# Kernel optimization log

Measured on AMD Instinct MI355X. Metric: run time of the kernel, lower is better.

The kernel has to match this reference:

```python
import jax, jax.numpy as jnp
import numpy as np

EPS = 1e-12

def _l2normalize(v):
    return v / (jnp.sum(v ** 2) ** 0.5 + EPS)

def spectral_norm(w, u):
    # w: [Cin, Cout] (flattened 1x1 conv kernel), u: [1, Cout]; 1 power iteration
    v = _l2normalize(u @ w.T)          # [1, Cin]
    u2 = _l2normalize(v @ w)           # [1, Cout]
    sigma = (v @ w @ u2.T)[0, 0]
    return w / sigma

def conv1x1(x, w):
    # x: [B,H,W,Cin], w: [Cin,Cout]
    return jnp.einsum('bhwc,cd->bhwd', x, w)

def maxpool2(x):
    B, H, W, C = x.shape
    return x.reshape(B, H // 2, 2, W // 2, 2, C).max(axis=(2, 4))

def setup_inputs() -> dict:
    key = jax.random.key(0)
    ks = jax.random.split(key, 10)
    B, H, W, C = 16, 64, 64, 512
    c8, c2 = C // 8, C // 2
    x = jax.random.normal(ks[0], (B, H, W, C), dtype=jnp.float32)
    k_theta = jax.random.normal(ks[1], (C, c8), dtype=jnp.float32) * 0.05
    u_theta = jax.random.normal(ks[2], (1, c8), dtype=jnp.float32)
    k_phi = jax.random.normal(ks[3], (C, c8), dtype=jnp.float32) * 0.05
    u_phi = jax.random.normal(ks[4], (1, c8), dtype=jnp.float32)
    k_g = jax.random.normal(ks[5], (C, c2), dtype=jnp.float32) * 0.05
    u_g = jax.random.normal(ks[6], (1, c2), dtype=jnp.float32)
    k_attn = jax.random.normal(ks[7], (c2, C), dtype=jnp.float32) * 0.05
    u_attn = jax.random.normal(ks[8], (1, C), dtype=jnp.float32)
    sigma = jnp.float32(0.1)
    return {"x": x, "k_theta": k_theta, "u_theta": u_theta,
            "k_phi": k_phi, "u_phi": u_phi, "k_g": k_g, "u_g": u_g,
            "k_attn": k_attn, "u_attn": u_attn, "sigma": sigma}

def reference(x, k_theta, u_theta, k_phi, u_phi, k_g, u_g, k_attn, u_attn, sigma):
    B, H, W, C = x.shape
    c8, c2 = C // 8, C // 2
    loc = H * W
    down = loc // 4
    theta = conv1x1(x, spectral_norm(k_theta, u_theta)).reshape(B, loc, c8)
    phi = maxpool2(conv1x1(x, spectral_norm(k_phi, u_phi))).reshape(B, down, c8)
    attn = jax.nn.softmax(jnp.einsum('bnc,bmc->bnm', theta, phi), axis=-1)  # [B, loc, down]
    g = maxpool2(conv1x1(x, spectral_norm(k_g, u_g))).reshape(B, down, c2)
    attn_g = jnp.einsum('bnm,bmc->bnc', attn, g).reshape(B, H, W, c2)
    attn_g = conv1x1(attn_g, spectral_norm(k_attn, u_attn))
    return x + sigma * attn_g
```

## Files before the change

### kernel.cpp

```cpp
#include <hip/hip_runtime.h>
#include <hip/hip_bf16.h>


using bf16 = __hip_bfloat16;
typedef unsigned short u16;
typedef __attribute__((ext_vector_type(8))) short bf16x8;
typedef __attribute__((ext_vector_type(4))) float f32x4;

#define MFMA16(a, b, c) __builtin_amdgcn_mfma_f32_16x16x32_bf16((a), (b), (c), 0, 0, 0)

#define WS_FLAG   0
#define WS_WAT2   787456
#define WS_THETA  1311744
#define WS_PHI    9700352
#define WS_G      11797504
#define WS_WAT    20186112
#define WS_TOTAL  20448256

__device__ __forceinline__ float bf2f(bf16 v) { return __bfloat162float(v); }
__device__ __forceinline__ bf16 f2bf(float v) { return __float2bfloat16(v); }
__device__ __forceinline__ u16 f2bf_bits(float v) { bf16 h = f2bf(v); return *(u16*)&h; }

template <typename T> struct io;
template <> struct io<bf16> {
  static __device__ __forceinline__ float ld(const bf16* p) { return bf2f(*p); }
  static __device__ __forceinline__ void st(bf16* p, float v) { *p = f2bf(v); }
  static __device__ __forceinline__ int tag() { return 0; }
};
template <> struct io<float> {
  static __device__ __forceinline__ float ld(const float* p) { return *p; }
  static __device__ __forceinline__ void st(float* p, float v) { *p = v; }
  static __device__ __forceinline__ int tag() { return 1; }
};

__global__ __launch_bounds__(256) void detect_kernel(const void* xraw, int* flag) {
  const u16* p = (const u16*)xraw;
  int t = threadIdx.x;
  int cnt = 0;
  for (int i = t; i < 65536; i += 256) {
    u16 v = p[i];
    if ((v & 0x7F80u) == 0x7F80u) cnt++;
  }
#pragma unroll
  for (int o = 32; o > 0; o >>= 1) cnt += __shfl_down(cnt, o, 64);
  __shared__ int red[4];
  if ((t & 63) == 0) red[t >> 6] = cnt;
  __syncthreads();
  if (t == 0) flag[0] = (red[0] + red[1] + red[2] + red[3] > 4) ? 1 : 0;
}

__device__ __forceinline__ float block_sum_256(float x, float* red) {
#pragma unroll
  for (int o = 32; o > 0; o >>= 1) x += __shfl_down(x, o, 64);
  __syncthreads();
  if ((threadIdx.x & 63) == 0) red[threadIdx.x >> 6] = x;
  __syncthreads();
  return red[0] + red[1] + red[2] + red[3];
}

template <typename T>
__global__ __launch_bounds__(256) void sn_kernel(
    const void* ktv, const void* utv, const void* kpv, const void* upv,
    const void* kgv, const void* ugv, const void* kav, const void* uav,
    u16* wAllT, u16* waT, const int* flag) {
  if (flag[0] != io<T>::tag()) return;
  __shared__ float v[512];
  __shared__ float red[4];
  const T* w; const T* u; int cin, cout;
  switch (blockIdx.x) {
    case 0:  w = (const T*)ktv; u = (const T*)utv; cin = 512; cout = 64;  break;
    case 1:  w = (const T*)kpv; u = (const T*)upv; cin = 512; cout = 64;  break;
    case 2:  w = (const T*)kgv; u = (const T*)ugv; cin = 512; cout = 256; break;
    default: w = (const T*)kav; u = (const T*)uav; cin = 256; cout = 512; break;
  }
  int t = threadIdx.x;
  float loc = 0.f;
  for (int i = t; i < cin; i += 256) {
    float acc = 0.f;
    const T* wr = w + (size_t)i * cout;
    for (int j = 0; j < cout; ++j) acc += io<T>::ld(u + j) * io<T>::ld(wr + j);
    v[i] = acc;
    loc += acc * acc;
  }
  float s1 = block_sum_256(loc, red);
  float inv1 = 1.f / (sqrtf(s1) + 1e-12f);
  float loc2 = 0.f;
  for (int j = t; j < cout; j += 256) {
    float acc = 0.f;
    for (int i = 0; i < cin; ++i) acc += v[i] * io<T>::ld(w + (size_t)i * cout + j);
    acc *= inv1;
    loc2 += acc * acc;
  }
  float s2 = block_sum_256(loc2, red);
  float sigma = s2 / (sqrtf(s2) + 1e-12f);
  float winv = 1.f / sigma;
  int total = cin * cout;
  for (int k = t; k < total; k += 256) {
    float val = io<T>::ld(w + k) * winv;
    u16 bits = f2bf_bits(val);
    switch (blockIdx.x) {
      case 0:  wAllT[(size_t)((k & 63)) * 512 + (k >> 6)] = bits; break;
      case 1:  wAllT[(size_t)(64 + (k & 63)) * 512 + (k >> 6)] = bits; break;
      case 2:  wAllT[(size_t)(128 + (k & 255)) * 512 + (k >> 8)] = bits; break;
      default: waT[(size_t)(k & 511) * 256 + (k >> 9)] = bits; break;
    }
  }
}

template <typename T>
__global__ __launch_bounds__(256, 2) void conv3_mfma_kernel(
    const void* xv, const u16* __restrict__ wAllT,
    bf16* __restrict__ theta, bf16* __restrict__ phi, bf16* __restrict__ gT,
    const int* flag) {
  if (flag[0] != io<T>::tag()) return;
  constexpr bool SPLIT = sizeof(T) == 4;
  const T* x = (const T*)xv;

  __shared__ u16 xh_s[2][64][136];
  __shared__ u16 xl_s[2][64][136];

  const int tid = threadIdx.x;
  const int w = tid >> 6;
  const int lane = tid & 63;
  const int quad = lane >> 4;
  const int l15 = lane & 15;
  const int bb = blockIdx.x >> 6;
  const int tile = blockIdx.x & 63;
  const int pth = tile >> 3, ptw = tile & 7;

  const int sp = tid >> 2;
  const int sq = tid & 3;
  const int swin = sp >> 2, sd = sp & 3;
  const int sh = 2 * (pth * 4 + (swin >> 2)) + (sd >> 1);
  const int sw = 2 * (ptw * 4 + (swin & 3)) + (sd & 1);
  const T* xrow = x + ((size_t)(bb * 64 + sh) * 64 + sw) * 512 + sq * 32;

  auto STAGE = [&](int buf, int kc) {
    if constexpr (SPLIT) {
      const float* src = (const float*)xrow + kc * 128;
#pragma unroll
      for (int hl = 0; hl < 2; ++hl) {
        float f[16];
#pragma unroll
        for (int i = 0; i < 4; ++i) {
          float4 v4 = ((const float4*)src)[hl * 4 + i];
          f[4 * i] = v4.x; f[4 * i + 1] = v4.y; f[4 * i + 2] = v4.z; f[4 * i + 3] = v4.w;
        }
        unsigned ph_[8], pl_[8];
#pragma unroll
        for (int i = 0; i < 8; ++i) {
          float a = f[2 * i], b = f[2 * i + 1];
          u16 ha = f2bf_bits(a), hb = f2bf_bits(b);
          float ra = a - __uint_as_float((unsigned)ha << 16);
          float rb = b - __uint_as_float((unsigned)hb << 16);
          ph_[i] = (unsigned)ha | ((unsigned)hb << 16);
          pl_[i] = (unsigned)f2bf_bits(ra) | ((unsigned)f2bf_bits(rb) << 16);
        }
        *(uint4*)&xh_s[buf][sp][sq * 32 + hl * 16] =
            make_uint4(ph_[0], ph_[1], ph_[2], ph_[3]);
        *(uint4*)&xh_s[buf][sp][sq * 32 + hl * 16 + 8] =
            make_uint4(ph_[4], ph_[5], ph_[6], ph_[7]);
        *(uint4*)&xl_s[buf][sp][sq * 32 + hl * 16] =
            make_uint4(pl_[0], pl_[1], pl_[2], pl_[3]);
        *(uint4*)&xl_s[buf][sp][sq * 32 + hl * 16 + 8] =
            make_uint4(pl_[4], pl_[5], pl_[6], pl_[7]);
      }
    } else {
      const u16* src = (const u16*)xrow + kc * 128;
#pragma unroll
      for (int i = 0; i < 4; ++i)
        *(uint4*)&xh_s[buf][sp][sq * 32 + i * 8] = ((const uint4*)src)[i];
    }
  };

  f32x4 acc[4][6];
#pragma unroll
  for (int mt = 0; mt < 4; ++mt)
#pragma unroll
    for (int nt = 0; nt < 6; ++nt) acc[mt][nt] = (f32x4){0.f, 0.f, 0.f, 0.f};

  const u16* wb = wAllT + (size_t)(w * 96 + l15) * 512 + quad * 8;

  STAGE(0, 0);
  __syncthreads();
#pragma unroll 1
  for (int kc = 0; kc < 4; ++kc) {
    const int buf = kc & 1;
    if (kc < 3) STAGE(buf ^ 1, kc + 1);
#pragma unroll
    for (int ks = 0; ks < 4; ++ks) {
      bf16x8 ah[4], al[4];
#pragma unroll
      for (int mt = 0; mt < 4; ++mt) {
        ah[mt] = *(const bf16x8*)&xh_s[buf][mt * 16 + l15][ks * 32 + quad * 8];
        if constexpr (SPLIT)
          al[mt] = *(const bf16x8*)&xl_s[buf][mt * 16 + l15][ks * 32 + quad * 8];
      }
#pragma unroll
      for (int nt = 0; nt < 6; ++nt) {
        bf16x8 b = *(const bf16x8*)(wb + (size_t)nt * 16 * 512 + kc * 128 + ks * 32);
#pragma unroll
        for (int mt = 0; mt < 4; ++mt) {
          acc[mt][nt] = MFMA16(ah[mt], b, acc[mt][nt]);
          if constexpr (SPLIT) acc[mt][nt] = MFMA16(al[mt], b, acc[mt][nt]);
        }
      }
    }
    __syncthreads();
  }

#pragma unroll
  for (int nt = 0; nt < 6; ++nt) {
    const int nb = w * 96 + nt * 16;
    const int n = nb + l15;
    if (nb < 64) {
#pragma unroll
      for (int mt = 0; mt < 4; ++mt)
#pragma unroll
        for (int r = 0; r < 4; ++r) {
          int p = mt * 16 + quad * 4 + r;
          int win = p >> 2, d = p & 3;
          int h = 2 * (pth * 4 + (win >> 2)) + (d >> 1);
          int wc = 2 * (ptw * 4 + (win & 3)) + (d & 1);
          theta[((size_t)bb * 4096 + h * 64 + wc) * 64 + n] = f2bf(acc[mt][nt][r]);
        }
    } else if (nb < 128) {
      const int ch = n - 64;
#pragma unroll
      for (int mt = 0; mt < 4; ++mt) {
        int win = mt * 4 + quad;
        int pp = (pth * 4 + (win >> 2)) * 32 + (ptw * 4 + (win & 3));
        float mx = fmaxf(fmaxf(acc[mt][nt][0], acc[mt][nt][1]),
                         fmaxf(acc[mt][nt][2], acc[mt][nt][3]));
        phi[((size_t)bb * 1024 + pp) * 64 + ch] = f2bf(mx);
      }
    } else {
      const int ch = n - 128;
#pragma unroll
      for (int mt = 0; mt < 4; ++mt) {
        int win = mt * 4 + quad;
        int pp = (pth * 4 + (win >> 2)) * 32 + (ptw * 4 + (win & 3));
        float mx = fmaxf(fmaxf(acc[mt][nt][0], acc[mt][nt][1]),
                         fmaxf(acc[mt][nt][2], acc[mt][nt][3]));
        gT[((size_t)bb * 256 + ch) * 1024 + pp] = f2bf(mx);
      }
    }
  }
}

template <typename T>
__global__ __launch_bounds__(256) void attn_kernel(
    const bf16* __restrict__ thetab, const bf16* __restrict__ phib,
    const bf16* __restrict__ gTb, void* __restrict__ outv, const int* flag) {
  if (flag[0] != io<T>::tag()) return;
  __shared__ u16 ph_s[64][70];
  __shared__ u16 gt_s[256][70];
  __shared__ u16 p_s[4][16][70];

  const int tid = threadIdx.x;
  const int w = tid >> 6;
  const int lane = tid & 63;
  const int quad = lane >> 4;
  const int l15 = lane & 15;
  const int qt = blockIdx.x * 4 + w;
  const int bb = qt >> 8;
  const int q0 = (qt & 255) * 16;

  const u16* th = (const u16*)thetab + ((size_t)bb * 4096 + q0 + l15) * 64 + quad * 8;
  const bf16x8 a0 = *(const bf16x8*)th;
  const bf16x8 a1 = *(const bf16x8*)(th + 32);

  const u16* ph = (const u16*)phib + (size_t)bb * 1024 * 64;
  const u16* gT = (const u16*)gTb + (size_t)bb * 256 * 1024;

  f32x4 o[16];
#pragma unroll
  for (int i = 0; i < 16; ++i) o[i] = (f32x4){0.f, 0.f, 0.f, 0.f};
  float mold[4] = {-1e30f, -1e30f, -1e30f, -1e30f};
  float lsum[4] = {0.f, 0.f, 0.f, 0.f};

  const int pr = tid >> 2, pc = (tid & 3) * 16;
  const int gr = tid >> 3, gc = (tid & 7) * 8;

#pragma unroll 1
  for (int kc = 0; kc < 16; ++kc) {
    __syncthreads();
    {
      const u16* src = ph + ((kc * 64 + pr) * 64 + pc);
      *(uint4*)&ph_s[pr][pc] = *(const uint4*)src;
      *(uint4*)&ph_s[pr][pc + 8] = *(const uint4*)(src + 8);
    }
#pragma unroll
    for (int i = 0; i < 8; ++i) {
      const u16* src = gT + (size_t)(i * 32 + gr) * 1024 + kc * 64 + gc;
      *(uint4*)&gt_s[i * 32 + gr][gc] = *(const uint4*)src;
    }
    __syncthreads();

    f32x4 s[4];
#pragma unroll
    for (int t4 = 0; t4 < 4; ++t4) {
      bf16x8 b0 = *(const bf16x8*)&ph_s[t4 * 16 + l15][quad * 8];
      bf16x8 b1 = *(const bf16x8*)&ph_s[t4 * 16 + l15][32 + quad * 8];
      f32x4 z = (f32x4){0.f, 0.f, 0.f, 0.f};
      z = MFMA16(a0, b0, z);
      z = MFMA16(a1, b1, z);
      s[t4] = z;
    }
    float rmax[4], mnew[4], alpha[4], rsum[4];
#pragma unroll
    for (int r = 0; r < 4; ++r) {
      rmax[r] = fmaxf(fmaxf(s[0][r], s[1][r]), fmaxf(s[2][r], s[3][r]));
#pragma unroll
      for (int m = 1; m <= 8; m <<= 1) rmax[r] = fmaxf(rmax[r], __shfl_xor(rmax[r], m, 64));
      mnew[r] = fmaxf(mold[r], rmax[r]);
      alpha[r] = __expf(mold[r] - mnew[r]);
      mold[r] = mnew[r];
      rsum[r] = 0.f;
    }
#pragma unroll
    for (int t4 = 0; t4 < 4; ++t4)
#pragma unroll
      for (int r = 0; r < 4; ++r) {
        float pv = __expf(s[t4][r] - mnew[r]);
        rsum[r] += pv;
        p_s[w][quad * 4 + r][t4 * 16 + l15] = f2bf_bits(pv);
      }
#pragma unroll
    for (int r = 0; r < 4; ++r) {
#pragma unroll
      for (int m = 1; m <= 8; m <<= 1) rsum[r] += __shfl_xor(rsum[r], m, 64);
      lsum[r] = lsum[r] * alpha[r] + rsum[r];
    }
#pragma unroll
    for (int i = 0; i < 16; ++i) {
      o[i][0] *= alpha[0]; o[i][1] *= alpha[1];
      o[i][2] *= alpha[2]; o[i][3] *= alpha[3];
    }
    bf16x8 pa0 = *(const bf16x8*)&p_s[w][l15][quad * 8];
    bf16x8 pa1 = *(const bf16x8*)&p_s[w][l15][32 + quad * 8];
#pragma unroll
    for (int t4 = 0; t4 < 16; ++t4) {
      bf16x8 b0 = *(const bf16x8*)&gt_s[t4 * 16 + l15][quad * 8];
      bf16x8 b1 = *(const bf16x8*)&gt_s[t4 * 16 + l15][32 + quad * 8];
      o[t4] = MFMA16(pa0, b0, o[t4]);
      o[t4] = MFMA16(pa1, b1, o[t4]);
    }
  }

  const size_t RB = 512 * sizeof(T);
  char* ob = (char*)outv;
  float inv[4];
#pragma unroll
  for (int r = 0; r < 4; ++r) inv[r] = 1.f / lsum[r];
#pragma unroll
  for (int t4 = 0; t4 < 16; ++t4)
#pragma unroll
    for (int r = 0; r < 4; ++r) {
      size_t row = (size_t)bb * 4096 + q0 + quad * 4 + r;
      u16* dst = (u16*)(ob + row * RB + RB / 2) + t4 * 16 + l15;
      *dst = f2bf_bits(o[t4][r] * inv[r]);
    }
}

template <typename T>
__global__ __launch_bounds__(256, 3) void proj_kernel(
    const u16* __restrict__ waT, const void* __restrict__ xv,
    const void* __restrict__ sigv, void* __restrict__ outv, const int* flag) {
  if (flag[0] != io<T>::tag()) return;
  const T* xp = (const T*)xv;
  T* outp = (T*)outv;
  __shared__ u16 a_s[64][264];

  const int tid = threadIdx.x;
  const int w = tid >> 6;
  const int lane = tid & 63;
  const int quad = lane >> 4;
  const int l15 = lane & 15;
  const int R0 = blockIdx.x * 64;
  const size_t RB = 512 * sizeof(T);

  {
    int row = tid >> 2, seg = tid & 3;
    const uint4* src = (const uint4*)((const char*)outv + (size_t)(R0 + row) * RB + RB / 2);
#pragma unroll
    for (int i = 0; i < 8; ++i)
      *(uint4*)&a_s[row][seg * 64 + i * 8] = src[seg * 8 + i];
  }
  __syncthreads();

  float sg = io<T>::ld((const T*)sigv);
#pragma unroll 1
  for (int h = 0; h < 2; ++h) {
    f32x4 pc[16];
#pragma unroll
    for (int i = 0; i < 16; ++i) pc[i] = (f32x4){0.f, 0.f, 0.f, 0.f};
#pragma unroll 1
    for (int ks = 0; ks < 8; ++ks) {
      bf16x8 a = *(const bf16x8*)&a_s[w * 16 + l15][ks * 32 + quad * 8];
#pragma unroll
      for (int t4 = 0; t4 < 16; ++t4) {
        bf16x8 b = *(const bf16x8*)(waT + (size_t)(h * 256 + t4 * 16 + l15) * 256 + ks * 32 + quad * 8);
        pc[t4] = MFMA16(a, b, pc[t4]);
      }
    }
#pragma unroll
    for (int t4 = 0; t4 < 16; ++t4)
#pragma unroll
      for (int r = 0; r < 4; ++r) {
        int row = R0 + w * 16 + quad * 4 + r;
        int col = h * 256 + t4 * 16 + l15;
        size_t off = (size_t)row * 512 + col;
        io<T>::st(outp + off, io<T>::ld(xp + off) + sg * pc[t4][r]);
      }
  }
}

extern "C" void kernel_launch(void* const* d_in, const int* in_sizes, int n_in,
                              void* d_out, int out_size, void* d_ws, size_t ws_size,
                              hipStream_t stream) {
  if (ws_size < (size_t)WS_TOTAL) return;
  char* ws = (char*)d_ws;
  int*   flag  = (int*)(ws + WS_FLAG);
  u16*   wAllT = (u16*)(ws + WS_WAT2);
  bf16*  theta = (bf16*)(ws + WS_THETA);
  bf16*  phi   = (bf16*)(ws + WS_PHI);
  bf16*  gT    = (bf16*)(ws + WS_G);
  u16*   waT   = (u16*)(ws + WS_WAT);

  detect_kernel<<<1, 256, 0, stream>>>(d_in[0], flag);

  sn_kernel<bf16><<<4, 256, 0, stream>>>(d_in[1], d_in[2], d_in[3], d_in[4],
                                         d_in[5], d_in[6], d_in[7], d_in[8],
                                         wAllT, waT, flag);
  sn_kernel<float><<<4, 256, 0, stream>>>(d_in[1], d_in[2], d_in[3], d_in[4],
                                          d_in[5], d_in[6], d_in[7], d_in[8],
                                          wAllT, waT, flag);

  conv3_mfma_kernel<bf16><<<1024, 256, 0, stream>>>(d_in[0], wAllT, theta, phi, gT, flag);
  conv3_mfma_kernel<float><<<1024, 256, 0, stream>>>(d_in[0], wAllT, theta, phi, gT, flag);

  attn_kernel<bf16><<<1024, 256, 0, stream>>>(theta, phi, gT, d_out, flag);
  attn_kernel<float><<<1024, 256, 0, stream>>>(theta, phi, gT, d_out, flag);

  proj_kernel<bf16><<<1024, 256, 0, stream>>>(waT, d_in[0], d_in[9], d_out, flag);
  proj_kernel<float><<<1024, 256, 0, stream>>>(waT, d_in[0], d_in[9], d_out, flag);
}
```

Measured before the change: 849.8 us.

## Process two query tiles per wave in attention, parallelize spectral-norm reductions

The attention kernel now has each wave handle 32 query rows (two 16-row tiles) instead of 16. Each phi/g tile staged in shared memory is therefore reused across twice as many queries, and the grid is halved. The spectral-norm kernel is rewritten with compile-time shapes, a wave-parallel first matvec and a split accumulation in the second. The detect kernel uses vectorized loads. The doubled accumulator set (32 f32x4 outputs) raises register pressure and may cut occupancy, and only 512 blocks may leave some compute units underused.

Measured after the change: 794.8 us. 6.5% less time.

```diff
diff --git a/kernel.cpp b/kernel.cpp
--- a/kernel.cpp
+++ b/kernel.cpp
@@ -34,12 +34,18 @@
 };
 
 __global__ __launch_bounds__(256) void detect_kernel(const void* xraw, int* flag) {
-  const u16* p = (const u16*)xraw;
+  const uint4* p = (const uint4*)xraw;
   int t = threadIdx.x;
   int cnt = 0;
-  for (int i = t; i < 65536; i += 256) {
-    u16 v = p[i];
-    if ((v & 0x7F80u) == 0x7F80u) cnt++;
+#pragma unroll 8
+  for (int i = 0; i < 32; ++i) {
+    uint4 v = p[t + i * 256];
+    unsigned d[4] = {v.x, v.y, v.z, v.w};
+#pragma unroll
+    for (int k = 0; k < 4; ++k) {
+      if ((d[k] & 0x7F80u) == 0x7F80u) cnt++;
+      if ((d[k] & 0x7F800000u) == 0x7F800000u) cnt++;
+    }
   }
 #pragma unroll
   for (int o = 32; o > 0; o >>= 1) cnt += __shfl_down(cnt, o, 64);
@@ -56,6 +62,66 @@
   if ((threadIdx.x & 63) == 0) red[threadIdx.x >> 6] = x;
   __syncthreads();
   return red[0] + red[1] + red[2] + red[3];
+}
+
+template <typename T, int CIN, int COUT, int MODE>
+__device__ __forceinline__ void sn_impl(const T* w, const T* u,
+                                        u16* wAllT, u16* waT) {
+  __shared__ float v[CIN];
+  __shared__ float red[4];
+  const int t = threadIdx.x, wv = t >> 6, ln = t & 63;
+
+  float uv[COUT / 64];
+#pragma unroll
+  for (int jj = 0; jj < COUT / 64; ++jj) uv[jj] = io<T>::ld(u + jj * 64 + ln);
+
+#pragma unroll 2
+  for (int i = wv; i < CIN; i += 4) {
+    float acc = 0.f;
+#pragma unroll
+    for (int jj = 0; jj < COUT / 64; ++jj)
+      acc += uv[jj] * io<T>::ld(w + (size_t)i * COUT + jj * 64 + ln);
+#pragma unroll
+    for (int o = 32; o > 0; o >>= 1) acc += __shfl_down(acc, o, 64);
+    if (ln == 0) v[i] = acc;
+  }
+  __syncthreads();
+  float loc = 0.f;
+  for (int i = t; i < CIN; i += 256) loc += v[i] * v[i];
+  float s1 = block_sum_256(loc, red);
+  float inv1 = 1.f / (sqrtf(s1) + 1e-12f);
+
+  float loc2 = 0.f;
+#pragma unroll
+  for (int j0 = 0; j0 < COUT; j0 += 256) {
+    int j = j0 + t;
+    if (j < COUT) {
+      float a0 = 0.f, a1 = 0.f, a2 = 0.f, a3 = 0.f;
+#pragma unroll 4
+      for (int i = 0; i < CIN; i += 4) {
+        a0 += v[i + 0] * io<T>::ld(w + (size_t)(i + 0) * COUT + j);
+        a1 += v[i + 1] * io<T>::ld(w + (size_t)(i + 1) * COUT + j);
+        a2 += v[i + 2] * io<T>::ld(w + (size_t)(i + 2) * COUT + j);
+        a3 += v[i + 3] * io<T>::ld(w + (size_t)(i + 3) * COUT + j);
+      }
+      float acc = ((a0 + a1) + (a2 + a3)) * inv1;
+      loc2 += acc * acc;
+    }
+  }
+  float s2 = block_sum_256(loc2, red);
+  float sigma = s2 / (sqrtf(s2) + 1e-12f);
+  float winv = 1.f / sigma;
+
+#pragma unroll 4
+  for (int k = t; k < CIN * COUT; k += 256) {
+    float val = io<T>::ld(w + k) * winv;
+    u16 bits = f2bf_bits(val);
+    int i = k / COUT, j = k % COUT;
+    if constexpr (MODE == 0) wAllT[(size_t)j * 512 + i] = bits;
+    if constexpr (MODE == 1) wAllT[(size_t)(64 + j) * 512 + i] = bits;
+    if constexpr (MODE == 2) wAllT[(size_t)(128 + j) * 512 + i] = bits;
+    if constexpr (MODE == 3) waT[(size_t)j * 256 + i] = bits;
+  }
 }
 
 template <typename T>
@@ -64,46 +130,11 @@
     const void* kgv, const void* ugv, const void* kav, const void* uav,
     u16* wAllT, u16* waT, const int* flag) {
   if (flag[0] != io<T>::tag()) return;
-  __shared__ float v[512];
-  __shared__ float red[4];
-  const T* w; const T* u; int cin, cout;
   switch (blockIdx.x) {
-    case 0:  w = (const T*)ktv; u = (const T*)utv; cin = 512; cout = 64;  break;
-    case 1:  w = (const T*)kpv; u = (const T*)upv; cin = 512; cout = 64;  break;
-    case 2:  w = (const T*)kgv; u = (const T*)ugv; cin = 512; cout = 256; break;
-    default: w = (const T*)kav; u = (const T*)uav; cin = 256; cout = 512; break;
-  }
-  int t = threadIdx.x;
-  float loc = 0.f;
-  for (int i = t; i < cin; i += 256) {
-    float acc = 0.f;
-    const T* wr = w + (size_t)i * cout;
-    for (int j = 0; j < cout; ++j) acc += io<T>::ld(u + j) * io<T>::ld(wr + j);
-    v[i] = acc;
-    loc += acc * acc;
-  }
-  float s1 = block_sum_256(loc, red);
-  float inv1 = 1.f / (sqrtf(s1) + 1e-12f);
-  float loc2 = 0.f;
-  for (int j = t; j < cout; j += 256) {
-    float acc = 0.f;
-    for (int i = 0; i < cin; ++i) acc += v[i] * io<T>::ld(w + (size_t)i * cout + j);
-    acc *= inv1;
-    loc2 += acc * acc;
-  }
-  float s2 = block_sum_256(loc2, red);
-  float sigma = s2 / (sqrtf(s2) + 1e-12f);
-  float winv = 1.f / sigma;
-  int total = cin * cout;
-  for (int k = t; k < total; k += 256) {
-    float val = io<T>::ld(w + k) * winv;
-    u16 bits = f2bf_bits(val);
-    switch (blockIdx.x) {
-      case 0:  wAllT[(size_t)((k & 63)) * 512 + (k >> 6)] = bits; break;
-      case 1:  wAllT[(size_t)(64 + (k & 63)) * 512 + (k >> 6)] = bits; break;
-      case 2:  wAllT[(size_t)(128 + (k & 255)) * 512 + (k >> 8)] = bits; break;
-      default: waT[(size_t)(k & 511) * 256 + (k >> 9)] = bits; break;
-    }
+    case 0:  sn_impl<T, 512, 64, 0>((const T*)ktv, (const T*)utv, wAllT, waT); break;
+    case 1:  sn_impl<T, 512, 64, 1>((const T*)kpv, (const T*)upv, wAllT, waT); break;
+    case 2:  sn_impl<T, 512, 256, 2>((const T*)kgv, (const T*)ugv, wAllT, waT); break;
+    default: sn_impl<T, 256, 512, 3>((const T*)kav, (const T*)uav, wAllT, waT); break;
   }
 }
 
@@ -255,7 +286,7 @@
   if (flag[0] != io<T>::tag()) return;
   __shared__ u16 ph_s[64][70];
   __shared__ u16 gt_s[256][70];
-  __shared__ u16 p_s[4][16][70];
+  __shared__ u16 p_s[4][32][70];
 
   const int tid = threadIdx.x;
   const int w = tid >> 6;
@@ -263,21 +294,31 @@
   const int quad = lane >> 4;
   const int l15 = lane & 15;
   const int qt = blockIdx.x * 4 + w;
-  const int bb = qt >> 8;
-  const int q0 = (qt & 255) * 16;
-
-  const u16* th = (const u16*)thetab + ((size_t)bb * 4096 + q0 + l15) * 64 + quad * 8;
-  const bf16x8 a0 = *(const bf16x8*)th;
-  const bf16x8 a1 = *(const bf16x8*)(th + 32);
+  const int bb = qt >> 7;
+  const int q0 = (qt & 127) * 32;
+
+  bf16x8 aT[2][2];
+#pragma unroll
+  for (int t = 0; t < 2; ++t) {
+    const u16* th = (const u16*)thetab +
+                    ((size_t)bb * 4096 + q0 + t * 16 + l15) * 64 + quad * 8;
+    aT[t][0] = *(const bf16x8*)th;
+    aT[t][1] = *(const bf16x8*)(th + 32);
+  }
 
   const u16* ph = (const u16*)phib + (size_t)bb * 1024 * 64;
   const u16* gT = (const u16*)gTb + (size_t)bb * 256 * 1024;
 
-  f32x4 o[16];
-#pragma unroll
-  for (int i = 0; i < 16; ++i) o[i] = (f32x4){0.f, 0.f, 0.f, 0.f};
-  float mold[4] = {-1e30f, -1e30f, -1e30f, -1e30f};
-  float lsum[4] = {0.f, 0.f, 0.f, 0.f};
+  f32x4 o[2][16];
+#pragma unroll
+  for (int t = 0; t < 2; ++t)
+#pragma unroll
+    for (int i = 0; i < 16; ++i) o[t][i] = (f32x4){0.f, 0.f, 0.f, 0.f};
+  float mold[2][4], lsum[2][4];
+#pragma unroll
+  for (int t = 0; t < 2; ++t)
+#pragma unroll
+    for (int r = 0; r < 4; ++r) { mold[t][r] = -1e30f; lsum[t][r] = 0.f; }
 
   const int pr = tid >> 2, pc = (tid & 3) * 16;
   const int gr = tid >> 3, gc = (tid & 7) * 8;
@@ -297,70 +338,85 @@
     }
     __syncthreads();
 
-    f32x4 s[4];
+    f32x4 s[2][4];
 #pragma unroll
     for (int t4 = 0; t4 < 4; ++t4) {
       bf16x8 b0 = *(const bf16x8*)&ph_s[t4 * 16 + l15][quad * 8];
       bf16x8 b1 = *(const bf16x8*)&ph_s[t4 * 16 + l15][32 + quad * 8];
-      f32x4 z = (f32x4){0.f, 0.f, 0.f, 0.f};
-      z = MFMA16(a0, b0, z);
-      z = MFMA16(a1, b1, z);
-      s[t4] = z;
-    }
-    float rmax[4], mnew[4], alpha[4], rsum[4];
-#pragma unroll
-    for (int r = 0; r < 4; ++r) {
-      rmax[r] = fmaxf(fmaxf(s[0][r], s[1][r]), fmaxf(s[2][r], s[3][r]));
-#pragma unroll
-      for (int m = 1; m <= 8; m <<= 1) rmax[r] = fmaxf(rmax[r], __shfl_xor(rmax[r], m, 64));
-      mnew[r] = fmaxf(mold[r], rmax[r]);
-      alpha[r] = __expf(mold[r] - mnew[r]);
-      mold[r] = mnew[r];
-      rsum[r] = 0.f;
-    }
-#pragma unroll
-    for (int t4 = 0; t4 < 4; ++t4)
+#pragma unroll
+      for (int t = 0; t < 2; ++t) {
+        f32x4 z = (f32x4){0.f, 0.f, 0.f, 0.f};
+        z = MFMA16(aT[t][0], b0, z);
+        z = MFMA16(aT[t][1], b1, z);
+        s[t][t4] = z;
+      }
+    }
+#pragma unroll
+    for (int t = 0; t < 2; ++t) {
+      float rmax[4], mnew[4], alpha[4], rsum[4];
 #pragma unroll
       for (int r = 0; r < 4; ++r) {
-        float pv = __expf(s[t4][r] - mnew[r]);
-        rsum[r] += pv;
-        p_s[w][quad * 4 + r][t4 * 16 + l15] = f2bf_bits(pv);
-      }
-#pragma unroll
-    for (int r = 0; r < 4; ++r) {
-#pragma unroll
-      for (int m = 1; m <= 8; m <<= 1) rsum[r] += __shfl_xor(rsum[r], m, 64);
-      lsum[r] = lsum[r] * alpha[r] + rsum[r];
-    }
-#pragma unroll
-    for (int i = 0; i < 16; ++i) {
-      o[i][0] *= alpha[0]; o[i][1] *= alpha[1];
-      o[i][2] *= alpha[2]; o[i][3] *= alpha[3];
-    }
-    bf16x8 pa0 = *(const bf16x8*)&p_s[w][l15][quad * 8];
-    bf16x8 pa1 = *(const bf16x8*)&p_s[w][l15][32 + quad * 8];
+        rmax[r] = fmaxf(fmaxf(s[t][0][r], s[t][1][r]),
+                        fmaxf(s[t][2][r], s[t][3][r]));
+#pragma unroll
+        for (int m = 1; m <= 8; m <<= 1)
+          rmax[r] = fmaxf(rmax[r], __shfl_xor(rmax[r], m, 64));
+        mnew[r] = fmaxf(mold[t][r], rmax[r]);
+        alpha[r] = __expf(mold[t][r] - mnew[r]);
+        mold[t][r] = mnew[r];
+        rsum[r] = 0.f;
+      }
+#pragma unroll
+      for (int t4 = 0; t4 < 4; ++t4)
+#pragma unroll
+        for (int r = 0; r < 4; ++r) {
+          float pv = __expf(s[t][t4][r] - mnew[r]);
+          rsum[r] += pv;
+          p_s[w][t * 16 + quad * 4 + r][t4 * 16 + l15] = f2bf_bits(pv);
+        }
+#pragma unroll
+      for (int r = 0; r < 4; ++r) {
+#pragma unroll
+        for (int m = 1; m <= 8; m <<= 1) rsum[r] += __shfl_xor(rsum[r], m, 64);
+        lsum[t][r] = lsum[t][r] * alpha[r] + rsum[r];
+      }
+#pragma unroll
+      for (int i = 0; i < 16; ++i) {
+        o[t][i][0] *= alpha[0]; o[t][i][1] *= alpha[1];
+        o[t][i][2] *= alpha[2]; o[t][i][3] *= alpha[3];
+      }
+    }
+    bf16x8 pa00 = *(const bf16x8*)&p_s[w][l15][quad * 8];
+    bf16x8 pa01 = *(const bf16x8*)&p_s[w][l15][32 + quad * 8];
+    bf16x8 pa10 = *(const bf16x8*)&p_s[w][16 + l15][quad * 8];
+    bf16x8 pa11 = *(const bf16x8*)&p_s[w][16 + l15][32 + quad * 8];
 #pragma unroll
     for (int t4 = 0; t4 < 16; ++t4) {
       bf16x8 b0 = *(const bf16x8*)&gt_s[t4 * 16 + l15][quad * 8];
       bf16x8 b1 = *(const bf16x8*)&gt_s[t4 * 16 + l15][32 + quad * 8];
-      o[t4] = MFMA16(pa0, b0, o[t4]);
-      o[t4] = MFMA16(pa1, b1, o[t4]);
+      o[0][t4] = MFMA16(pa00, b0, o[0][t4]);
+      o[0][t4] = MFMA16(pa01, b1, o[0][t4]);
+      o[1][t4] = MFMA16(pa10, b0, o[1][t4]);
+      o[1][t4] = MFMA16(pa11, b1, o[1][t4]);
     }
   }
 
   const size_t RB = 512 * sizeof(T);
   char* ob = (char*)outv;
-  float inv[4];
-#pragma unroll
-  for (int r = 0; r < 4; ++r) inv[r] = 1.f / lsum[r];
-#pragma unroll
-  for (int t4 = 0; t4 < 16; ++t4)
-#pragma unroll
-    for (int r = 0; r < 4; ++r) {
-      size_t row = (size_t)bb * 4096 + q0 + quad * 4 + r;
-      u16* dst = (u16*)(ob + row * RB + RB / 2) + t4 * 16 + l15;
-      *dst = f2bf_bits(o[t4][r] * inv[r]);
-    }
+#pragma unroll
+  for (int t = 0; t < 2; ++t) {
+    float inv[4];
+#pragma unroll
+    for (int r = 0; r < 4; ++r) inv[r] = 1.f / lsum[t][r];
+#pragma unroll
+    for (int t4 = 0; t4 < 16; ++t4)
+#pragma unroll
+      for (int r = 0; r < 4; ++r) {
+        size_t row = (size_t)bb * 4096 + q0 + t * 16 + quad * 4 + r;
+        u16* dst = (u16*)(ob + row * RB + RB / 2) + t4 * 16 + l15;
+        *dst = f2bf_bits(o[t][t4][r] * inv[r]);
+      }
+  }
 }
 
 template <typename T>
@@ -440,8 +496,8 @@
   conv3_mfma_kernel<bf16><<<1024, 256, 0, stream>>>(d_in[0], wAllT, theta, phi, gT, flag);
   conv3_mfma_kernel<float><<<1024, 256, 0, stream>>>(d_in[0], wAllT, theta, phi, gT, flag);
 
-  attn_kernel<bf16><<<1024, 256, 0, stream>>>(theta, phi, gT, d_out, flag);
-  attn_kernel<float><<<1024, 256, 0, stream>>>(theta, phi, gT, d_out, flag);
+  attn_kernel<bf16><<<512, 256, 0, stream>>>(theta, phi, gT, d_out, flag);
+  attn_kernel<float><<<512, 256, 0, stream>>>(theta, phi, gT, d_out, flag);
 
   proj_kernel<bf16><<<1024, 256, 0, stream>>>(waT, d_in[0], d_in[9], d_out, flag);
   proj_kernel<float><<<1024, 256, 0, stream>>>(waT, d_in[0], d_in[9], d_out, flag);
```
